# Kernel optimization log

Hardware: AMD Instinct MI355X
Metric: run time of the kernel (lower is better)

## Reference

```python
import jax, jax.numpy as jnp
import numpy as np

P = 10  # pred_num_conn (capped by max_pred_num_conn), component 0 = background
L = 6   # label_num_conn, component 0 = background
N, H, W = 4, 1024, 1024


def setup_inputs() -> dict:
    key = jax.random.key(0)
    k1, k2, k3 = jax.random.split(key, 3)
    pred = jax.random.uniform(k1, (N, H, W), dtype=jnp.float32)
    pred_conn = jax.random.randint(k2, (N, H, W), 0, P, dtype=jnp.int32)
    label_conn = jax.random.randint(k3, (N, H, W), 0, L, dtype=jnp.int32)
    return {"pred": pred, "pred_conn": pred_conn, "label_conn": label_conn}


def _image_sc_loss(pred_i, pconn, lconn):
    # pred_i: [H,W] float, pconn/lconn: [H,W] int component ids
    ph = jax.nn.one_hot(pconn, P, dtype=pred_i.dtype)   # [H,W,P]
    lh = jax.nn.one_hot(lconn, L, dtype=pred_i.dtype)   # [H,W,L]
    pm = ph * pred_i[..., None]                          # pred_j = mask_j * pred
    inter = jnp.einsum('hwl,hwp->lp', lh, pm)            # [L,P] intersection areas
    pred_area = jnp.sum(pm, axis=(0, 1))                 # [P]
    label_area = jnp.sum(lh, axis=(0, 1))                # [L]
    union = label_area[:, None] + pred_area[None, :] - inter
    safe_union = jnp.where(union == 0, 1.0, union)
    # compute_iou: 0 if intersect==0, 1 if union==0, else inter/union
    iou = jnp.where(inter == 0, 0.0,
                    jnp.where(union == 0, 1.0, inter / safe_union))
    ious = iou[1:, 1:]                                   # drop background comps -> [L-1, P-1]
    pair_conn = jnp.sum(ious, axis=1)                    # sum of nonzero ious per label comp
    pair_num = jnp.sum(ious != 0, axis=1).astype(pred_i.dtype)
    contrib = jnp.where(pair_num > 0,
                        pair_conn / jnp.where(pair_num > 0, pair_num, 1.0), 0.0)
    pair_conn_sum = jnp.sum(contrib)
    pred_col_sum = jnp.sum(ious, axis=0)                 # [P-1]
    lone_pred_num = jnp.sum(pred_col_sum == 0).astype(pred_i.dtype)
    real_label_num = jnp.asarray(L - 1, pred_i.dtype)
    img_connectivity = pair_conn_sum / (real_label_num + lone_pred_num)
    return 1.0 - img_connectivity                        # sc_loss for one class (class_num=1)


def reference(pred, pred_conn, label_conn):
    sc = jax.vmap(_image_sc_loss)(pred, pred_conn, label_conn)  # [N]
    return jnp.mean(sc)
```

## Files before the change

kernel.cpp:

```cpp
#include <hip/hip_runtime.h>

#define PP 10
#define LL 6
#define NIMG 4
#define HW (1024*1024)
#define NBO 59
#define BINS 60
#define BX 256
#define TPB 256
#define ITERS 4


__global__ __launch_bounds__(TPB) void accum_kernel(
    const float* __restrict__ pred,
    const int*   __restrict__ pconn,
    const int*   __restrict__ lconn,
    float*       __restrict__ ws)
{
    __shared__ float ld[NBO * 64];

    const int tid = threadIdx.x;
    const int img = blockIdx.y;
    const size_t base = (size_t)img * HW;

    const float4* __restrict__ p4  = (const float4*)(pred  + base);
    const int4*   __restrict__ pc4 = (const int4*)(pconn + base);
    const int4*   __restrict__ lc4 = (const int4*)(lconn + base);

    const int v0 = blockIdx.x * TPB + tid;
    const int stride = BX * TPB;

    float A[45];
    float PA[9];
    float CNT[5];
#pragma unroll
    for (int i = 0; i < 45; ++i) A[i] = 0.0f;
#pragma unroll
    for (int i = 0; i < 9; ++i) PA[i] = 0.0f;
#pragma unroll
    for (int i = 0; i < 5; ++i) CNT[i] = 0.0f;

    float4 pcur = p4[v0];
    int4   pccur = pc4[v0];
    int4   lccur = lc4[v0];

#pragma unroll
    for (int i = 0; i < ITERS; ++i) {
        float4 pnxt; int4 pcnxt, lcnxt;
        if (i + 1 < ITERS) {
            const int v = v0 + (i + 1) * stride;
            pnxt  = p4[v];
            pcnxt = pc4[v];
            lcnxt = lc4[v];
        }
#pragma unroll
        for (int c = 0; c < 4; ++c) {
            const float pv  = (c == 0) ? pcur.x  : (c == 1) ? pcur.y  : (c == 2) ? pcur.z  : pcur.w;
            const int   lcv = (c == 0) ? lccur.x : (c == 1) ? lccur.y : (c == 2) ? lccur.z : lccur.w;
            const int   pcv = (c == 0) ? pccur.x : (c == 1) ? pccur.y : (c == 2) ? pccur.z : pccur.w;

            float op[PP];
#pragma unroll
            for (int q = 1; q < PP; ++q) op[q] = (pcv == q) ? 1.0f : 0.0f;
#pragma unroll
            for (int q = 1; q < PP; ++q) PA[q - 1] = fmaf(pv, op[q], PA[q - 1]);
#pragma unroll
            for (int l = 1; l < LL; ++l) {
                const bool ol = (lcv == l);
                CNT[l - 1] += ol ? 1.0f : 0.0f;
                const float hl = ol ? pv : 0.0f;
#pragma unroll
                for (int q = 1; q < PP; ++q)
                    A[(l - 1) * 9 + (q - 1)] = fmaf(hl, op[q], A[(l - 1) * 9 + (q - 1)]);
            }
        }
        pcur = pnxt; pccur = pcnxt; lccur = lcnxt;
    }

    const int unit = (tid >> 6) * 16 + ((tid & 63) >> 2);
    const bool writer = ((tid & 3) == 0);
#pragma unroll
    for (int b = 0; b < 45; ++b) {
        float s = A[b];
        s += __shfl_down(s, 1, 64); s += __shfl_down(s, 2, 64);
        if (writer) ld[b * 64 + unit] = s;
    }
#pragma unroll
    for (int b = 0; b < 9; ++b) {
        float s = PA[b];
        s += __shfl_down(s, 1, 64); s += __shfl_down(s, 2, 64);
        if (writer) ld[(45 + b) * 64 + unit] = s;
    }
#pragma unroll
    for (int b = 0; b < 5; ++b) {
        float s = CNT[b];
        s += __shfl_down(s, 1, 64); s += __shfl_down(s, 2, 64);
        if (writer) ld[(54 + b) * 64 + unit] = s;
    }
    __syncthreads();

    if (tid < NBO) {
        const float4* row = (const float4*)(ld + tid * 64);
        float s = 0.0f;
#pragma unroll
        for (int i = 0; i < 16; ++i) {
            const float4 t4 = row[(i + tid) & 15];
            s += t4.x + t4.y + t4.z + t4.w;
        }
        ws[((size_t)img * BX + blockIdx.x) * BINS + tid] = s;
    }
}

__global__ __launch_bounds__(1024) void finalize_kernel(
    const float* __restrict__ ws, float* __restrict__ out)
{
    __shared__ float part[4][NIMG * BINS];
    __shared__ float red[NIMG * BINS];
    __shared__ float contrib[NIMG];
    const int t = threadIdx.x;

    for (int T = t; T < 4 * NIMG * BINS; T += 1024) {
        const int ib = T >> 2, sub = T & 3;
        const int img = ib / BINS, b = ib % BINS;
        float s = 0.0f;
        if (b < NBO) {
            const float* basep = ws + ((size_t)img * BX + sub) * BINS + b;
#pragma unroll 8
            for (int j = 0; j < BX / 4; ++j) s += basep[(size_t)j * 4 * BINS];
        }
        part[sub][ib] = s;
    }
    __syncthreads();

    if (t < NIMG * BINS)
        red[t] = part[0][t] + part[1][t] + part[2][t] + part[3][t];
    __syncthreads();

    if (t < NIMG) {
        const float* b = red + t * BINS;
        float colsum[9];
#pragma unroll
        for (int p = 0; p < 9; ++p) colsum[p] = 0.0f;
        float pair_conn_sum = 0.0f;
        for (int l = 0; l < 5; ++l) {
            const float la = b[54 + l];
            float pc = 0.0f; int pn = 0;
            for (int p = 0; p < 9; ++p) {
                const float in = b[l * 9 + p];
                const float un = la + b[45 + p] - in;
                float iou;
                if (in == 0.0f)      iou = 0.0f;
                else if (un == 0.0f) iou = 1.0f;
                else                 iou = in / un;
                colsum[p] += iou;
                pc += iou;
                pn += (iou != 0.0f) ? 1 : 0;
            }
            if (pn > 0) pair_conn_sum += pc / (float)pn;
        }
        int lone = 0;
        for (int p = 0; p < 9; ++p) lone += (colsum[p] == 0.0f) ? 1 : 0;
        contrib[t] = 1.0f - pair_conn_sum / (5.0f + (float)lone);
    }
    __syncthreads();
    if (t == 0)
        out[0] = (contrib[0] + contrib[1] + contrib[2] + contrib[3]) * 0.25f;
}

extern "C" void kernel_launch(void* const* d_in, const int* in_sizes, int n_in,
                              void* d_out, int out_size, void* d_ws, size_t ws_size,
                              hipStream_t stream) {
    const float* pred  = (const float*)d_in[0];
    const int*   pconn = (const int*)d_in[1];
    const int*   lconn = (const int*)d_in[2];
    float* out = (float*)d_out;
    float* ws  = (float*)d_ws;

    dim3 grid(BX, NIMG);
    accum_kernel<<<grid, TPB, 0, stream>>>(pred, pconn, lconn, ws);

    finalize_kernel<<<1, 1024, 0, stream>>>(ws, out);
}
```

Before: 112.5 us.

## Transpose workspace layout for vectorized finalize reduction and drop manual prefetch

The per-block partial sums are now stored bin-major, so each bin's 256 block partials sit contiguously. The finalize kernel can then read them with float4 loads, four threads per bin, and combine the four with shuffles, replacing strided scalar loads and a second shared-memory pass. The accumulation kernel drops its manual register double-buffering in favour of plain per-iteration loads and adds a min-blocks-per-SM launch bound to cap register use and raise occupancy. The launch bound risks register spills given the 59 accumulators each thread holds.

```diff
diff --git a/kernel.cpp b/kernel.cpp
--- a/kernel.cpp
+++ b/kernel.cpp
@@ -5,13 +5,12 @@
 #define NIMG 4
 #define HW (1024*1024)
 #define NBO 59
-#define BINS 60
 #define BX 256
 #define TPB 256
 #define ITERS 4
 
 
-__global__ __launch_bounds__(TPB) void accum_kernel(
+__global__ __launch_bounds__(TPB, 4) void accum_kernel(
     const float* __restrict__ pred,
     const int*   __restrict__ pconn,
     const int*   __restrict__ lconn,
@@ -40,24 +39,17 @@
 #pragma unroll
     for (int i = 0; i < 5; ++i) CNT[i] = 0.0f;
 
-    float4 pcur = p4[v0];
-    int4   pccur = pc4[v0];
-    int4   lccur = lc4[v0];
-
 #pragma unroll
     for (int i = 0; i < ITERS; ++i) {
-        float4 pnxt; int4 pcnxt, lcnxt;
-        if (i + 1 < ITERS) {
-            const int v = v0 + (i + 1) * stride;
-            pnxt  = p4[v];
-            pcnxt = pc4[v];
-            lcnxt = lc4[v];
-        }
+        const int v = v0 + i * stride;
+        const float4 p  = p4[v];
+        const int4   pc = pc4[v];
+        const int4   lc = lc4[v];
 #pragma unroll
         for (int c = 0; c < 4; ++c) {
-            const float pv  = (c == 0) ? pcur.x  : (c == 1) ? pcur.y  : (c == 2) ? pcur.z  : pcur.w;
-            const int   lcv = (c == 0) ? lccur.x : (c == 1) ? lccur.y : (c == 2) ? lccur.z : lccur.w;
-            const int   pcv = (c == 0) ? pccur.x : (c == 1) ? pccur.y : (c == 2) ? pccur.z : pccur.w;
+            const float pv  = (c == 0) ? p.x  : (c == 1) ? p.y  : (c == 2) ? p.z  : p.w;
+            const int   lcv = (c == 0) ? lc.x : (c == 1) ? lc.y : (c == 2) ? lc.z : lc.w;
+            const int   pcv = (c == 0) ? pc.x : (c == 1) ? pc.y : (c == 2) ? pc.z : pc.w;
 
             float op[PP];
 #pragma unroll
@@ -74,7 +66,6 @@
                     A[(l - 1) * 9 + (q - 1)] = fmaf(hl, op[q], A[(l - 1) * 9 + (q - 1)]);
             }
         }
-        pcur = pnxt; pccur = pcnxt; lccur = lcnxt;
     }
 
     const int unit = (tid >> 6) * 16 + ((tid & 63) >> 2);
@@ -107,37 +98,34 @@
             const float4 t4 = row[(i + tid) & 15];
             s += t4.x + t4.y + t4.z + t4.w;
         }
-        ws[((size_t)img * BX + blockIdx.x) * BINS + tid] = s;
+        ws[((size_t)img * NBO + tid) * BX + blockIdx.x] = s;
     }
 }
 
 __global__ __launch_bounds__(1024) void finalize_kernel(
     const float* __restrict__ ws, float* __restrict__ out)
 {
-    __shared__ float part[4][NIMG * BINS];
-    __shared__ float red[NIMG * BINS];
+    __shared__ float red[NIMG * NBO];
     __shared__ float contrib[NIMG];
     const int t = threadIdx.x;
 
-    for (int T = t; T < 4 * NIMG * BINS; T += 1024) {
-        const int ib = T >> 2, sub = T & 3;
-        const int img = ib / BINS, b = ib % BINS;
+    const int row = t >> 2, q = t & 3;
+    if (row < NIMG * NBO) {
+        const float4* basep = (const float4*)(ws + (size_t)row * BX + q * 64);
         float s = 0.0f;
-        if (b < NBO) {
-            const float* basep = ws + ((size_t)img * BX + sub) * BINS + b;
-#pragma unroll 8
-            for (int j = 0; j < BX / 4; ++j) s += basep[(size_t)j * 4 * BINS];
+#pragma unroll
+        for (int i = 0; i < 16; ++i) {
+            const float4 v = basep[i];
+            s += v.x + v.y + v.z + v.w;
         }
-        part[sub][ib] = s;
+        s += __shfl_down(s, 1, 64);
+        s += __shfl_down(s, 2, 64);
+        if (q == 0) red[row] = s;
     }
     __syncthreads();
 
-    if (t < NIMG * BINS)
-        red[t] = part[0][t] + part[1][t] + part[2][t] + part[3][t];
-    __syncthreads();
-
     if (t < NIMG) {
-        const float* b = red + t * BINS;
+        const float* b = red + t * NBO;
         float colsum[9];
 #pragma unroll
         for (int p = 0; p < 9; ++p) colsum[p] = 0.0f;
```

After: 206.7 us. 1.84x slower.
